# Kernel optimization log

Measured on AMD Instinct MI355X. Metric: run time of the kernel, lower is better.

Reference implementation:

```python
import jax, jax.numpy as jnp
import numpy as np

B, S_DIM, A_DIM = 8192, 39, 4
D_IN = S_DIM + A_DIM  # 43
F = 1024              # n_features width
E = 8                 # n_experts
C = 10                # n_contexts
N_OUT = 1


def setup_inputs() -> dict:
    key = jax.random.key(0)
    ks = jax.random.split(key, 12)
    inp = {
        "state": jax.random.normal(ks[0], (B, S_DIM), jnp.float32),
        "action": jax.random.normal(ks[1], (B, A_DIM), jnp.float32),
        "c": jax.random.randint(ks[2], (B,), 0, C, jnp.int32),
        # per-expert backbone params (InputLayer+ParallelLayer => E independent MLPs)
        "W0": jax.random.normal(ks[3], (E, D_IN, F), jnp.float32) * 0.05,
        "b0": jnp.zeros((E, F), jnp.float32),
        "W1": jax.random.normal(ks[4], (E, F, F), jnp.float32) * 0.03,
        "b1": jnp.zeros((E, F), jnp.float32),
        # task encoder: Linear(n_contexts -> n_experts, bias=False), weight [E, C]
        "Wte": jax.random.normal(ks[5], (E, C), jnp.float32) * 0.3,
        # per-context output heads: Linear(F -> 1)
        "Wh": jax.random.normal(ks[6], (C, F, N_OUT), jnp.float32) * 0.03,
        "bh": jnp.zeros((C, N_OUT), jnp.float32),
    }
    return inp


def reference(state, action, c, W0, b0, W1, b1, Wte, Wh, bh):
    # mixture weights: one_hot(c) @ Wte^T  ==  Wte[:, c]^T  -> [B, E]
    w = Wte.T[c]                                            # [B, E]
    sa = jnp.concatenate([state, action], axis=1)           # [B, D_IN]
    # per-expert backbone MLP (ReLU after each layer, incl. last since activation='ReLU')
    h = jax.nn.relu(jnp.einsum('bi,eio->ebo', sa, W0) + b0[:, None, :])   # [E, B, F]
    h = jax.nn.relu(jnp.einsum('ebi,eio->ebo', h, W1) + b1[:, None, :])   # [E, B, F]
    feats = jnp.transpose(h, (1, 0, 2))                     # [B, E, F]
    feats = jax.nn.relu(feats)                              # agg_activation[0]
    mixed = jnp.einsum('be,bef->bf', w, feats)              # [B, F]
    mixed = jax.nn.relu(mixed)                              # agg_activation[1]
    # context-routed heads: gather each sample's head params (same math as the
    # unique-context scatter loop in the original)
    q = jnp.einsum('bf,bfo->bo', mixed, Wh[c]) + bh[c]      # [B, 1]
    return jnp.squeeze(q, axis=-1)                          # [B]
```

## Files before the change

kernel.cpp:

```cpp
#include <hip/hip_runtime.h>
#include <hip/hip_bf16.h>
#include <stdint.h>

typedef __attribute__((ext_vector_type(8))) __bf16 bf16x8;
typedef __attribute__((ext_vector_type(4))) float f32x4;

__device__ __forceinline__ unsigned short f2b(float f) {
    return __builtin_bit_cast(unsigned short, __float2bfloat16(f));
}

__device__ __forceinline__ void gload_lds16(const void* g, void* l) {
    __builtin_amdgcn_global_load_lds(
        (__attribute__((address_space(1))) void*)(uintptr_t)g,
        (__attribute__((address_space(3))) void*)l,
        16, 0, 0);
}

#define MFMA16(a, b, c) __builtin_amdgcn_mfma_f32_16x16x32_bf16((a), (b), (c), 0, 0, 0)


__global__ void k_prep_sa(const float* __restrict__ state, const float* __restrict__ action,
                          const int* __restrict__ c, const float* __restrict__ Wte,
                          unsigned short* __restrict__ SA, float* __restrict__ wmix, int B) {
    int b = blockIdx.x * 256 + threadIdx.x;
    if (b >= B) return;
    unsigned short* row = SA + (size_t)b * 64;
#pragma unroll
    for (int i = 0; i < 39; ++i) row[i] = f2b(state[(size_t)b * 39 + i]);
#pragma unroll
    for (int i = 0; i < 4; ++i) row[39 + i] = f2b(action[(size_t)b * 4 + i]);
#pragma unroll
    for (int i = 43; i < 64; ++i) row[i] = 0;
    int ctx = c[b];
#pragma unroll
    for (int e = 0; e < 8; ++e) wmix[(size_t)b * 8 + e] = Wte[e * 10 + ctx];
}

__global__ void k_prep_w0t(const float* __restrict__ W0, unsigned short* __restrict__ W0T) {
    int idx = blockIdx.x * 256 + threadIdx.x;
    int e = idx >> 10, f = idx & 1023;
    unsigned short* dst = W0T + (size_t)idx * 64;
#pragma unroll 1
    for (int k = 0; k < 43; ++k) dst[k] = f2b(W0[((size_t)e * 43 + k) * 1024 + f]);
#pragma unroll
    for (int k = 43; k < 64; ++k) dst[k] = 0;
}

__global__ void k_prep_w1t(const float* __restrict__ W1, unsigned short* __restrict__ W1T) {
    __shared__ float t[64][65];
    int k0 = blockIdx.x * 64, n0 = blockIdx.y * 64, e = blockIdx.z;
    int tid = threadIdx.x;
    int cl = tid & 63;
    int rg = tid >> 6;
    const float* src = W1 + ((size_t)e * 1024 + k0) * 1024 + n0;
#pragma unroll
    for (int i = 0; i < 16; ++i) {
        int kr = rg * 16 + i;
        t[kr][cl] = src[(size_t)kr * 1024 + cl];
    }
    __syncthreads();
    int nl = tid >> 2, kg = tid & 3;
    unsigned short* dst = W1T + ((size_t)e * 1024 + n0 + nl) * 1024 + k0 + kg * 16;
#pragma unroll
    for (int j = 0; j < 16; ++j) dst[j] = f2b(t[kg * 16 + j][nl]);
}

__global__ __launch_bounds__(256, 2)
void k_layer0(const unsigned short* __restrict__ SA,
              const unsigned short* __restrict__ W0T,
              const float* __restrict__ b0,
              unsigned short* __restrict__ H0,
              int Bc, int row0) {
    __shared__ unsigned short As[128 * 64];
    __shared__ unsigned short Bs[128 * 64];
    int bm = blockIdx.x, bn = blockIdx.y, e = blockIdx.z;
    int tid = threadIdx.x, lane = tid & 63;
    int wv = tid >> 6, wr = wv >> 1, wc = wv & 1;
    int l15 = lane & 15, kg = lane >> 4;

    const char* Ag = (const char*)(SA + (size_t)(row0 + bm * 128) * 64);
    const char* Bg = (const char*)(W0T + ((size_t)e * 1024 + bn * 128) * 64);
#pragma unroll
    for (int it = 0; it < 4; ++it) {
        int off = tid * 16 + it * 4096;
        gload_lds16(Ag + off, (char*)As + off);
        gload_lds16(Bg + off, (char*)Bs + off);
    }
    __syncthreads();

    f32x4 acc[4][4];
#pragma unroll
    for (int mi = 0; mi < 4; ++mi)
#pragma unroll
        for (int ni = 0; ni < 4; ++ni) acc[mi][ni] = (f32x4)0.0f;

#pragma unroll
    for (int ks = 0; ks < 2; ++ks) {
        bf16x8 af[4], bv[4];
#pragma unroll
        for (int mi = 0; mi < 4; ++mi)
            af[mi] = *(const bf16x8*)&As[(wr * 64 + mi * 16 + l15) * 64 + ks * 32 + kg * 8];
#pragma unroll
        for (int ni = 0; ni < 4; ++ni)
            bv[ni] = *(const bf16x8*)&Bs[(wc * 64 + ni * 16 + l15) * 64 + ks * 32 + kg * 8];
#pragma unroll
        for (int mi = 0; mi < 4; ++mi)
#pragma unroll
            for (int ni = 0; ni < 4; ++ni)
                acc[mi][ni] = MFMA16(af[mi], bv[ni], acc[mi][ni]);
    }

    float b0v[4];
#pragma unroll
    for (int ni = 0; ni < 4; ++ni)
        b0v[ni] = b0[e * 1024 + bn * 128 + wc * 64 + ni * 16 + l15];
#pragma unroll
    for (int mi = 0; mi < 4; ++mi)
#pragma unroll
        for (int ni = 0; ni < 4; ++ni)
#pragma unroll
            for (int j = 0; j < 4; ++j) {
                int rloc = bm * 128 + wr * 64 + mi * 16 + kg * 4 + j;
                int col = bn * 128 + wc * 64 + ni * 16 + l15;
                float h = fmaxf(acc[mi][ni][j] + b0v[ni], 0.0f);
                H0[((size_t)e * Bc + rloc) * 1024 + col] = f2b(h);
            }
}

__global__ __launch_bounds__(512, 2)
void k_layer1_mix(const unsigned short* __restrict__ H0,
                  const unsigned short* __restrict__ W1T,
                  const float* __restrict__ b1,
                  const float* __restrict__ wmix,
                  float* __restrict__ mixed,
                  int Bc, int row0) {
    __shared__ unsigned short As[2][256 * 64];
    __shared__ unsigned short Bs[2][128 * 64];
    __shared__ float wmixLds[256 * 8];
    __shared__ float b1Lds[8 * 128];

    int nwg = (Bc / 256) * 8;
    int wg = blockIdx.x;
    int cpx = nwg >> 3;
    int swz = (wg & 7) * cpx + (wg >> 3);
    int bm = swz >> 3, bn = swz & 7;

    int tid = threadIdx.x, lane = tid & 63;
    int wv = tid >> 6;
    int wr = wv >> 1, wc = wv & 1;
    int l15 = lane & 15, kg = lane >> 4;

    int tid16 = tid * 16;
    int aSrc[4], aDst[4], bSrc[2], bDst[2];
#pragma unroll
    for (int i = 0; i < 4; ++i) {
        int flat = tid16 + i * 8192;
        int row = flat >> 7, colb = flat & 127;
        aDst[i] = flat;
        aSrc[i] = row * 2048 + (colb ^ ((row & 7) << 4));
    }
#pragma unroll
    for (int i = 0; i < 2; ++i) {
        int flat = tid16 + i * 8192;
        int row = flat >> 7, colb = flat & 127;
        bDst[i] = flat;
        bSrc[i] = row * 2048 + (colb ^ ((row & 7) << 4));
    }

    const char* h0base = (const char*)H0 + (size_t)(bm * 256) * 2048;
    const char* w1base = (const char*)W1T + (size_t)(bn * 128) * 2048;
    size_t eAstride = (size_t)Bc * 2048;

    int xsw = (l15 & 7) << 4;
    int aRow[4], bRow[4];
#pragma unroll
    for (int mi = 0; mi < 4; ++mi) aRow[mi] = (wr * 64 + mi * 16 + l15) * 128;
#pragma unroll
    for (int ni = 0; ni < 4; ++ni) bRow[ni] = (wc * 64 + ni * 16 + l15) * 128;
    int kg16 = kg * 16;

    for (int idx = tid; idx < 2048; idx += 512) {
        int r = idx >> 3, e = idx & 7;
        wmixLds[idx] = wmix[(size_t)(row0 + bm * 256 + r) * 8 + e];
    }
#pragma unroll
    for (int idx = tid; idx < 1024; idx += 512)
        b1Lds[idx] = b1[(idx >> 7) * 1024 + bn * 128 + (idx & 127)];
    __syncthreads();

    f32x4 acc[4][4], mix[4][4];
#pragma unroll
    for (int mi = 0; mi < 4; ++mi)
#pragma unroll
        for (int ni = 0; ni < 4; ++ni) { acc[mi][ni] = (f32x4)0.0f; mix[mi][ni] = (f32x4)0.0f; }

    const int NT = 128;

    auto STAGE = [&](int tt) {
        int e = tt >> 4;
        int k0b = (tt & 15) << 7;
        const char* Ab = h0base + (size_t)e * eAstride + k0b;
        const char* Bb = w1base + (size_t)e * (1024 * 2048) + k0b;
        char* Ad = (char*)As[tt & 1];
        char* Bd = (char*)Bs[tt & 1];
#pragma unroll
        for (int i = 0; i < 4; ++i) gload_lds16(Ab + aSrc[i], Ad + aDst[i]);
#pragma unroll
        for (int i = 0; i < 2; ++i) gload_lds16(Bb + bSrc[i], Bd + bDst[i]);
    };

    STAGE(0);

    for (int t = 0; t < NT; ++t) {
        if (t + 1 < NT) {
            STAGE(t + 1);
            asm volatile("s_waitcnt vmcnt(6)\n\ts_barrier" ::: "memory");
        } else {
            asm volatile("s_waitcnt vmcnt(0)\n\ts_barrier" ::: "memory");
        }
        __builtin_amdgcn_sched_barrier(0);

        const char* Ab = (const char*)As[t & 1];
        const char* Bb = (const char*)Bs[t & 1];

        __builtin_amdgcn_s_setprio(1);
#pragma unroll
        for (int ks = 0; ks < 2; ++ks) {
            int kb = (ks * 64 + kg16) ^ xsw;
            bf16x8 af[4], bv[4];
#pragma unroll
            for (int mi = 0; mi < 4; ++mi) af[mi] = *(const bf16x8*)(Ab + aRow[mi] + kb);
#pragma unroll
            for (int ni = 0; ni < 4; ++ni) bv[ni] = *(const bf16x8*)(Bb + bRow[ni] + kb);
#pragma unroll
            for (int mi = 0; mi < 4; ++mi)
#pragma unroll
                for (int ni = 0; ni < 4; ++ni)
                    acc[mi][ni] = MFMA16(af[mi], bv[ni], acc[mi][ni]);
        }
        __builtin_amdgcn_s_setprio(0);
        __builtin_amdgcn_sched_barrier(0);
        asm volatile("s_waitcnt lgkmcnt(0)\n\ts_barrier" ::: "memory");

        if ((t & 15) == 15) {
            int e = t >> 4;
            float b1v[4];
#pragma unroll
            for (int ni = 0; ni < 4; ++ni)
                b1v[ni] = b1Lds[e * 128 + wc * 64 + ni * 16 + l15];
#pragma unroll
            for (int mi = 0; mi < 4; ++mi)
#pragma unroll
                for (int j = 0; j < 4; ++j) {
                    int lrow = wr * 64 + mi * 16 + kg * 4 + j;
                    float w = wmixLds[lrow * 8 + e];
#pragma unroll
                    for (int ni = 0; ni < 4; ++ni) {
                        float h = fmaxf(acc[mi][ni][j] + b1v[ni], 0.0f);
                        mix[mi][ni][j] += w * h;
                        acc[mi][ni][j] = 0.0f;
                    }
                }
        }
    }

#pragma unroll
    for (int mi = 0; mi < 4; ++mi)
#pragma unroll
        for (int ni = 0; ni < 4; ++ni)
#pragma unroll
            for (int j = 0; j < 4; ++j) {
                int lrow = wr * 64 + mi * 16 + kg * 4 + j;
                int col = bn * 128 + wc * 64 + ni * 16 + l15;
                mixed[(size_t)(bm * 256 + lrow) * 1024 + col] = fmaxf(mix[mi][ni][j], 0.0f);
            }
}

__global__ void k_head(const float* __restrict__ mixed, const float* __restrict__ Wh,
                       const float* __restrict__ bh, const int* __restrict__ c,
                       float* __restrict__ q, int Bc, int row0) {
    int row = blockIdx.x * 4 + (threadIdx.x >> 6);
    int lane = threadIdx.x & 63;
    if (row >= Bc) return;
    int grow = row0 + row;
    int ctx = c[grow];
    const float4* m4 = (const float4*)(mixed + (size_t)row * 1024);
    const float4* w4 = (const float4*)(Wh + (size_t)ctx * 1024);
    float s = 0.0f;
#pragma unroll
    for (int i = 0; i < 4; ++i) {
        float4 a = m4[lane + i * 64];
        float4 b = w4[lane + i * 64];
        s += a.x * b.x + a.y * b.y + a.z * b.z + a.w * b.w;
    }
#pragma unroll
    for (int off = 32; off > 0; off >>= 1) s += __shfl_down(s, off);
    if (lane == 0) q[grow] = s + bh[ctx];
}

extern "C" void kernel_launch(void* const* d_in, const int* in_sizes, int n_in,
                              void* d_out, int out_size, void* d_ws, size_t ws_size,
                              hipStream_t stream) {
    const float* state  = (const float*)d_in[0];
    const float* action = (const float*)d_in[1];
    const int*   c      = (const int*)d_in[2];
    const float* W0     = (const float*)d_in[3];
    const float* b0     = (const float*)d_in[4];
    const float* W1     = (const float*)d_in[5];
    const float* b1     = (const float*)d_in[6];
    const float* Wte    = (const float*)d_in[7];
    const float* Wh     = (const float*)d_in[8];
    const float* bh     = (const float*)d_in[9];
    float* q = (float*)d_out;
    int B = in_sizes[2];

    char* p = (char*)d_ws;
    unsigned short* W1T = (unsigned short*)p; p += (size_t)8 * 1024 * 1024 * 2;
    unsigned short* W0T = (unsigned short*)p; p += (size_t)8 * 1024 * 64 * 2;
    unsigned short* SA  = (unsigned short*)p; p += (size_t)B * 64 * 2;
    float* wmix         = (float*)p;          p += (size_t)B * 8 * 4;
    size_t fixed = (size_t)(p - (char*)d_ws);

    int Bc = B;
    while (Bc > 256 && fixed + (size_t)Bc * (8 * 1024 * 2 + 1024 * 4) > ws_size) Bc >>= 1;

    unsigned short* H0 = (unsigned short*)p; p += (size_t)8 * Bc * 1024 * 2;
    float* mixed       = (float*)p;

    k_prep_sa<<<(B + 255) / 256, 256, 0, stream>>>(state, action, c, Wte, SA, wmix, B);
    k_prep_w0t<<<(8 * 1024) / 256, 256, 0, stream>>>(W0, W0T);
    k_prep_w1t<<<dim3(16, 16, 8), 256, 0, stream>>>(W1, W1T);

    for (int row0 = 0; row0 < B; row0 += Bc) {
        k_layer0<<<dim3(Bc / 128, 8, 8), 256, 0, stream>>>(SA, W0T, b0, H0, Bc, row0);
        k_layer1_mix<<<(Bc / 256) * 8, 512, 0, stream>>>(H0, W1T, b1, wmix, mixed, Bc, row0);
        k_head<<<(Bc + 3) / 4, 256, 0, stream>>>(mixed, Wh, bh, c, q, Bc, row0);
    }
}
```

Measured before the change: 233.6 us.

## Remap waves to 2x4 layout and split tile loads into interleaved phases

Changes the wave layout from 4x2 (64x64 per wave) to 2x4 (128x32 per wave). The stage loads are split into two groups, and the second half of A is issued mid-iteration, so global-to-LDS copies overlap with MFMA phases. Each phase now loads only a few A fragments and waits before its MFMAs, with a barrier per phase. The goal is to cut register pressure and expose load latency less, at the cost of more barriers and more A-fragment LDS reads per wave.

```diff
diff --git a/kernel.cpp b/kernel.cpp
--- a/kernel.cpp
+++ b/kernel.cpp
@@ -147,8 +147,10 @@
 
     int tid = threadIdx.x, lane = tid & 63;
     int wv = tid >> 6;
-    int wr = wv >> 1, wc = wv & 1;
+    int wr = wv >> 2, wc = wv & 3;
     int l15 = lane & 15, kg = lane >> 4;
+    int kg16 = kg * 16;
+    int xsw = (l15 & 7) << 4;
 
     int tid16 = tid * 16;
     int aSrc[4], aDst[4], bSrc[2], bDst[2];
@@ -171,108 +173,142 @@
     const char* w1base = (const char*)W1T + (size_t)(bn * 128) * 2048;
     size_t eAstride = (size_t)Bc * 2048;
 
-    int xsw = (l15 & 7) << 4;
-    int aRow[4], bRow[4];
-#pragma unroll
-    for (int mi = 0; mi < 4; ++mi) aRow[mi] = (wr * 64 + mi * 16 + l15) * 128;
-#pragma unroll
-    for (int ni = 0; ni < 4; ++ni) bRow[ni] = (wc * 64 + ni * 16 + l15) * 128;
-    int kg16 = kg * 16;
+    int aOff[8], bOff[2];
+#pragma unroll
+    for (int m = 0; m < 8; ++m) aOff[m] = (wr * 128 + m * 16 + l15) * 128;
+#pragma unroll
+    for (int n = 0; n < 2; ++n) bOff[n] = (wc * 32 + n * 16 + l15) * 128;
 
     for (int idx = tid; idx < 2048; idx += 512) {
         int r = idx >> 3, e = idx & 7;
         wmixLds[idx] = wmix[(size_t)(row0 + bm * 256 + r) * 8 + e];
     }
-#pragma unroll
     for (int idx = tid; idx < 1024; idx += 512)
         b1Lds[idx] = b1[(idx >> 7) * 1024 + bn * 128 + (idx & 127)];
     __syncthreads();
 
-    f32x4 acc[4][4], mix[4][4];
-#pragma unroll
-    for (int mi = 0; mi < 4; ++mi)
-#pragma unroll
-        for (int ni = 0; ni < 4; ++ni) { acc[mi][ni] = (f32x4)0.0f; mix[mi][ni] = (f32x4)0.0f; }
+    f32x4 acc[8][2], mix[8][2];
+#pragma unroll
+    for (int m = 0; m < 8; ++m)
+#pragma unroll
+        for (int n = 0; n < 2; ++n) { acc[m][n] = (f32x4)0.0f; mix[m][n] = (f32x4)0.0f; }
 
     const int NT = 128;
 
-    auto STAGE = [&](int tt) {
+    auto STAGE_G0 = [&](int tt) {
         int e = tt >> 4;
         int k0b = (tt & 15) << 7;
         const char* Ab = h0base + (size_t)e * eAstride + k0b;
         const char* Bb = w1base + (size_t)e * (1024 * 2048) + k0b;
         char* Ad = (char*)As[tt & 1];
         char* Bd = (char*)Bs[tt & 1];
-#pragma unroll
-        for (int i = 0; i < 4; ++i) gload_lds16(Ab + aSrc[i], Ad + aDst[i]);
-#pragma unroll
-        for (int i = 0; i < 2; ++i) gload_lds16(Bb + bSrc[i], Bd + bDst[i]);
+        gload_lds16(Bb + bSrc[0], Bd + bDst[0]);
+        gload_lds16(Bb + bSrc[1], Bd + bDst[1]);
+        gload_lds16(Ab + aSrc[0], Ad + aDst[0]);
+        gload_lds16(Ab + aSrc[2], Ad + aDst[2]);
     };
-
-    STAGE(0);
-
+    auto STAGE_G1 = [&](int tt) {
+        int e = tt >> 4;
+        int k0b = (tt & 15) << 7;
+        const char* Ab = h0base + (size_t)e * eAstride + k0b;
+        char* Ad = (char*)As[tt & 1];
+        gload_lds16(Ab + aSrc[1], Ad + aDst[1]);
+        gload_lds16(Ab + aSrc[3], Ad + aDst[3]);
+    };
+
+#define KB0 ((0 * 64 + kg16) ^ xsw)
+#define KB1 ((1 * 64 + kg16) ^ xsw)
+
+#define PHASE(M0, M1)                                                       \
+    {                                                                       \
+        bf16x8 a00 = *(const bf16x8*)(Ab + aOff[M0] + KB0);                 \
+        bf16x8 a01 = *(const bf16x8*)(Ab + aOff[M0] + KB1);                 \
+        bf16x8 a10 = *(const bf16x8*)(Ab + aOff[M1] + KB0);                 \
+        bf16x8 a11 = *(const bf16x8*)(Ab + aOff[M1] + KB1);                 \
+        asm volatile("s_waitcnt lgkmcnt(0)" ::: "memory");                  \
+        __builtin_amdgcn_sched_barrier(0);                                  \
+        __builtin_amdgcn_s_setprio(1);                                      \
+        acc[M0][0] = MFMA16(a00, bf00, acc[M0][0]);                         \
+        acc[M0][1] = MFMA16(a00, bf10, acc[M0][1]);                         \
+        acc[M1][0] = MFMA16(a10, bf00, acc[M1][0]);                         \
+        acc[M1][1] = MFMA16(a10, bf10, acc[M1][1]);                         \
+        acc[M0][0] = MFMA16(a01, bf01, acc[M0][0]);                         \
+        acc[M0][1] = MFMA16(a01, bf11, acc[M0][1]);                         \
+        acc[M1][0] = MFMA16(a11, bf01, acc[M1][0]);                         \
+        acc[M1][1] = MFMA16(a11, bf11, acc[M1][1]);                         \
+        __builtin_amdgcn_s_setprio(0);                                      \
+        __builtin_amdgcn_sched_barrier(0);                                  \
+        asm volatile("s_barrier" ::: "memory");                             \
+    }
+
+    STAGE_G0(0);
+    STAGE_G1(0);
+
+#pragma unroll 1
     for (int t = 0; t < NT; ++t) {
+        const char* Ab = (const char*)As[t & 1];
+        const char* Bb = (const char*)Bs[t & 1];
+
         if (t + 1 < NT) {
-            STAGE(t + 1);
+            STAGE_G0(t + 1);
+            asm volatile("s_waitcnt vmcnt(6)\n\ts_barrier" ::: "memory");
+        } else {
+            asm volatile("s_waitcnt vmcnt(2)\n\ts_barrier" ::: "memory");
+        }
+        __builtin_amdgcn_sched_barrier(0);
+        bf16x8 bf00 = *(const bf16x8*)(Bb + bOff[0] + KB0);
+        bf16x8 bf01 = *(const bf16x8*)(Bb + bOff[0] + KB1);
+        bf16x8 bf10 = *(const bf16x8*)(Bb + bOff[1] + KB0);
+        bf16x8 bf11 = *(const bf16x8*)(Bb + bOff[1] + KB1);
+        PHASE(0, 1)
+
+        PHASE(2, 3)
+
+        if (t + 1 < NT) {
+            STAGE_G1(t + 1);
             asm volatile("s_waitcnt vmcnt(6)\n\ts_barrier" ::: "memory");
         } else {
             asm volatile("s_waitcnt vmcnt(0)\n\ts_barrier" ::: "memory");
         }
         __builtin_amdgcn_sched_barrier(0);
-
-        const char* Ab = (const char*)As[t & 1];
-        const char* Bb = (const char*)Bs[t & 1];
-
-        __builtin_amdgcn_s_setprio(1);
-#pragma unroll
-        for (int ks = 0; ks < 2; ++ks) {
-            int kb = (ks * 64 + kg16) ^ xsw;
-            bf16x8 af[4], bv[4];
-#pragma unroll
-            for (int mi = 0; mi < 4; ++mi) af[mi] = *(const bf16x8*)(Ab + aRow[mi] + kb);
-#pragma unroll
-            for (int ni = 0; ni < 4; ++ni) bv[ni] = *(const bf16x8*)(Bb + bRow[ni] + kb);
-#pragma unroll
-            for (int mi = 0; mi < 4; ++mi)
-#pragma unroll
-                for (int ni = 0; ni < 4; ++ni)
-                    acc[mi][ni] = MFMA16(af[mi], bv[ni], acc[mi][ni]);
-        }
-        __builtin_amdgcn_s_setprio(0);
-        __builtin_amdgcn_sched_barrier(0);
-        asm volatile("s_waitcnt lgkmcnt(0)\n\ts_barrier" ::: "memory");
+        PHASE(4, 5)
+
+        PHASE(6, 7)
 
         if ((t & 15) == 15) {
             int e = t >> 4;
-            float b1v[4];
-#pragma unroll
-            for (int ni = 0; ni < 4; ++ni)
-                b1v[ni] = b1Lds[e * 128 + wc * 64 + ni * 16 + l15];
-#pragma unroll
-            for (int mi = 0; mi < 4; ++mi)
+            float b1v[2];
+#pragma unroll
+            for (int n = 0; n < 2; ++n)
+                b1v[n] = b1Lds[e * 128 + wc * 32 + n * 16 + l15];
+#pragma unroll
+            for (int m = 0; m < 8; ++m)
 #pragma unroll
                 for (int j = 0; j < 4; ++j) {
-                    int lrow = wr * 64 + mi * 16 + kg * 4 + j;
+                    int lrow = wr * 128 + m * 16 + kg * 4 + j;
                     float w = wmixLds[lrow * 8 + e];
 #pragma unroll
-                    for (int ni = 0; ni < 4; ++ni) {
-                        float h = fmaxf(acc[mi][ni][j] + b1v[ni], 0.0f);
-                        mix[mi][ni][j] += w * h;
-                        acc[mi][ni][j] = 0.0f;
+                    for (int n = 0; n < 2; ++n) {
+                        float h = fmaxf(acc[m][n][j] + b1v[n], 0.0f);
+                        mix[m][n][j] += w * h;
+                        acc[m][n][j] = 0.0f;
                     }
                 }
         }
     }
-
-#pragma unroll
-    for (int mi = 0; mi < 4; ++mi)
-#pragma unroll
-        for (int ni = 0; ni < 4; ++ni)
+#undef PHASE
+#undef KB0
+#undef KB1
+
+#pragma unroll
+    for (int m = 0; m < 8; ++m)
+#pragma unroll
+        for (int n = 0; n < 2; ++n)
 #pragma unroll
             for (int j = 0; j < 4; ++j) {
-                int lrow = wr * 64 + mi * 16 + kg * 4 + j;
-                int col = bn * 128 + wc * 64 + ni * 16 + l15;
-                mixed[(size_t)(bm * 256 + lrow) * 1024 + col] = fmaxf(mix[mi][ni][j], 0.0f);
+                int lrow = wr * 128 + m * 16 + kg * 4 + j;
+                int col = bn * 128 + wc * 32 + n * 16 + l15;
+                mixed[(size_t)(bm * 256 + lrow) * 1024 + col] = fmaxf(mix[m][n][j], 0.0f);
             }
 }
 
```

After: 291.5 us. 24.7% more time.

## Split experts into two groups with 256x256 tiles and bf16 partial mixes

Applied to the files above, without the earlier changes.

The layer-1 GEMM now uses 256x256 output tiles, and the 8 experts are split into two groups of 4, each handled by a different workgroup. Each group writes a bf16 partial mixture, and the head kernel sums the two partials, applies ReLU and does the dot product. The goal is more data reuse per tile (fewer global loads of H0 and W1T per FLOP) and a half-width intermediate. Global loads are split into two halves interleaved with the MFMA blocks. Costs are higher register pressure (128 accumulators plus 128 mix floats per thread) at 512 threads, which may cut occupancy or spill, and bf16 rounding of the partial sums.

```diff
diff --git a/kernel.cpp b/kernel.cpp
--- a/kernel.cpp
+++ b/kernel.cpp
@@ -7,6 +7,9 @@
 
 __device__ __forceinline__ unsigned short f2b(float f) {
     return __builtin_bit_cast(unsigned short, __float2bfloat16(f));
+}
+__device__ __forceinline__ float b2f(unsigned int u) {
+    return __builtin_bit_cast(float, u << 16);
 }
 
 __device__ __forceinline__ void gload_lds16(const void* g, void* l) {
@@ -50,8 +53,7 @@
     __shared__ float t[64][65];
     int k0 = blockIdx.x * 64, n0 = blockIdx.y * 64, e = blockIdx.z;
     int tid = threadIdx.x;
-    int cl = tid & 63;
-    int rg = tid >> 6;
+    int cl = tid & 63, rg = tid >> 6;
     const float* src = W1 + ((size_t)e * 1024 + k0) * 1024 + n0;
 #pragma unroll
     for (int i = 0; i < 16; ++i) {
@@ -132,166 +134,200 @@
                   const unsigned short* __restrict__ W1T,
                   const float* __restrict__ b1,
                   const float* __restrict__ wmix,
-                  float* __restrict__ mixed,
+                  unsigned short* __restrict__ mixedP,
                   int Bc, int row0) {
     __shared__ unsigned short As[2][256 * 64];
-    __shared__ unsigned short Bs[2][128 * 64];
-    __shared__ float wmixLds[256 * 8];
-    __shared__ float b1Lds[8 * 128];
-
-    int nwg = (Bc / 256) * 8;
+    __shared__ unsigned short Bs[2][256 * 64];
+    __shared__ float wmixLds[256 * 4];
+    __shared__ float b1Lds[4 * 256];
+
+    int nbm = Bc / 256;
+    int P = nbm * 2;
     int wg = blockIdx.x;
-    int cpx = nwg >> 3;
-    int swz = (wg & 7) * cpx + (wg >> 3);
-    int bm = swz >> 3, bn = swz & 7;
+    int bm, bn, g;
+    if ((P & 7) == 0) {
+        int c8 = wg & 7, j = wg >> 3;
+        int p = c8 + 8 * (j >> 2);
+        bn = j & 3;
+        bm = p >> 1; g = p & 1;
+    } else {
+        bn = wg & 3; g = (wg >> 2) & 1; bm = wg >> 3;
+    }
 
     int tid = threadIdx.x, lane = tid & 63;
     int wv = tid >> 6;
-    int wr = wv >> 1, wc = wv & 1;
+    int wr = wv >> 2, wc = wv & 3;
     int l15 = lane & 15, kg = lane >> 4;
+    int kg16 = kg * 16;
+    int xsw = (l15 & 7) << 4;
 
     int tid16 = tid * 16;
-    int aSrc[4], aDst[4], bSrc[2], bDst[2];
+    int sSrc[4], sDst[4];
 #pragma unroll
     for (int i = 0; i < 4; ++i) {
         int flat = tid16 + i * 8192;
         int row = flat >> 7, colb = flat & 127;
-        aDst[i] = flat;
-        aSrc[i] = row * 2048 + (colb ^ ((row & 7) << 4));
-    }
-#pragma unroll
-    for (int i = 0; i < 2; ++i) {
-        int flat = tid16 + i * 8192;
-        int row = flat >> 7, colb = flat & 127;
-        bDst[i] = flat;
-        bSrc[i] = row * 2048 + (colb ^ ((row & 7) << 4));
+        sDst[i] = flat;
+        sSrc[i] = row * 2048 + (colb ^ ((row & 7) << 4));
     }
 
     const char* h0base = (const char*)H0 + (size_t)(bm * 256) * 2048;
-    const char* w1base = (const char*)W1T + (size_t)(bn * 128) * 2048;
+    const char* w1base = (const char*)W1T + (size_t)(bn * 256) * 2048;
     size_t eAstride = (size_t)Bc * 2048;
 
-    int xsw = (l15 & 7) << 4;
-    int aRow[4], bRow[4];
-#pragma unroll
-    for (int mi = 0; mi < 4; ++mi) aRow[mi] = (wr * 64 + mi * 16 + l15) * 128;
-#pragma unroll
-    for (int ni = 0; ni < 4; ++ni) bRow[ni] = (wc * 64 + ni * 16 + l15) * 128;
-    int kg16 = kg * 16;
-
-    for (int idx = tid; idx < 2048; idx += 512) {
-        int r = idx >> 3, e = idx & 7;
-        wmixLds[idx] = wmix[(size_t)(row0 + bm * 256 + r) * 8 + e];
-    }
-#pragma unroll
+    int aOff[8], bOff[4];
+#pragma unroll
+    for (int m = 0; m < 8; ++m) aOff[m] = (wr * 128 + m * 16 + l15) * 128;
+#pragma unroll
+    for (int n = 0; n < 4; ++n) bOff[n] = (wc * 64 + n * 16 + l15) * 128;
+
+    for (int idx = tid; idx < 1024; idx += 512) {
+        int r = idx >> 2, el = idx & 3;
+        wmixLds[idx] = wmix[(size_t)(row0 + bm * 256 + r) * 8 + g * 4 + el];
+    }
     for (int idx = tid; idx < 1024; idx += 512)
-        b1Lds[idx] = b1[(idx >> 7) * 1024 + bn * 128 + (idx & 127)];
-    __syncthreads();
-
-    f32x4 acc[4][4], mix[4][4];
-#pragma unroll
-    for (int mi = 0; mi < 4; ++mi)
-#pragma unroll
-        for (int ni = 0; ni < 4; ++ni) { acc[mi][ni] = (f32x4)0.0f; mix[mi][ni] = (f32x4)0.0f; }
-
-    const int NT = 128;
-
-    auto STAGE = [&](int tt) {
-        int e = tt >> 4;
+        b1Lds[idx] = b1[(g * 4 + (idx >> 8)) * 1024 + bn * 256 + (idx & 255)];
+
+    f32x4 acc[8], acc2[8];
+    f32x4 A0[8][4];
+    float mix[8][4][4];
+#pragma unroll
+    for (int m = 0; m < 8; ++m)
+#pragma unroll
+        for (int n = 0; n < 4; ++n) {
+            A0[m][n] = (f32x4)0.0f;
+#pragma unroll
+            for (int j = 0; j < 4; ++j) mix[m][n][j] = 0.0f;
+        }
+    (void)acc; (void)acc2;
+
+    const int NT = 64;
+
+    auto STAGE_G = [&](int tt, int half) {
+        int el = tt >> 4;
         int k0b = (tt & 15) << 7;
-        const char* Ab = h0base + (size_t)e * eAstride + k0b;
-        const char* Bb = w1base + (size_t)e * (1024 * 2048) + k0b;
+        const char* Ab = h0base + (size_t)(g * 4 + el) * eAstride + k0b;
+        const char* Bb = w1base + (size_t)(g * 4 + el) * (1024 * 2048) + k0b;
         char* Ad = (char*)As[tt & 1];
         char* Bd = (char*)Bs[tt & 1];
-#pragma unroll
-        for (int i = 0; i < 4; ++i) gload_lds16(Ab + aSrc[i], Ad + aDst[i]);
-#pragma unroll
-        for (int i = 0; i < 2; ++i) gload_lds16(Bb + bSrc[i], Bd + bDst[i]);
+        int i0 = half * 2;
+        gload_lds16(Ab + sSrc[i0], Ad + sDst[i0]);
+        gload_lds16(Ab + sSrc[i0 + 1], Ad + sDst[i0 + 1]);
+        gload_lds16(Bb + sSrc[i0], Bd + sDst[i0]);
+        gload_lds16(Bb + sSrc[i0 + 1], Bd + sDst[i0 + 1]);
     };
 
-    STAGE(0);
-
+    STAGE_G(0, 0);
+    STAGE_G(0, 1);
+    __syncthreads();
+
+#pragma unroll 1
     for (int t = 0; t < NT; ++t) {
-        if (t + 1 < NT) {
-            STAGE(t + 1);
-            asm volatile("s_waitcnt vmcnt(6)\n\ts_barrier" ::: "memory");
-        } else {
-            asm volatile("s_waitcnt vmcnt(0)\n\ts_barrier" ::: "memory");
-        }
-        __builtin_amdgcn_sched_barrier(0);
-
         const char* Ab = (const char*)As[t & 1];
         const char* Bb = (const char*)Bs[t & 1];
 
-        __builtin_amdgcn_s_setprio(1);
-#pragma unroll
-        for (int ks = 0; ks < 2; ++ks) {
-            int kb = (ks * 64 + kg16) ^ xsw;
-            bf16x8 af[4], bv[4];
-#pragma unroll
-            for (int mi = 0; mi < 4; ++mi) af[mi] = *(const bf16x8*)(Ab + aRow[mi] + kb);
-#pragma unroll
-            for (int ni = 0; ni < 4; ++ni) bv[ni] = *(const bf16x8*)(Bb + bRow[ni] + kb);
-#pragma unroll
-            for (int mi = 0; mi < 4; ++mi)
-#pragma unroll
-                for (int ni = 0; ni < 4; ++ni)
-                    acc[mi][ni] = MFMA16(af[mi], bv[ni], acc[mi][ni]);
-        }
-        __builtin_amdgcn_s_setprio(0);
-        __builtin_amdgcn_sched_barrier(0);
-        asm volatile("s_waitcnt lgkmcnt(0)\n\ts_barrier" ::: "memory");
+        {
+            int kb = kg16 ^ xsw;
+            bf16x8 af[8], bf[4];
+#pragma unroll
+            for (int m = 0; m < 8; ++m) af[m] = *(const bf16x8*)(Ab + aOff[m] + kb);
+#pragma unroll
+            for (int n = 0; n < 4; ++n) bf[n] = *(const bf16x8*)(Bb + bOff[n] + kb);
+            if (t + 1 < NT) STAGE_G(t + 1, 0);
+            asm volatile("s_waitcnt lgkmcnt(0)" ::: "memory");
+            __builtin_amdgcn_sched_barrier(0);
+            __builtin_amdgcn_s_setprio(1);
+#pragma unroll
+            for (int m = 0; m < 8; ++m)
+#pragma unroll
+                for (int n = 0; n < 4; ++n)
+                    A0[m][n] = MFMA16(af[m], bf[n], A0[m][n]);
+            __builtin_amdgcn_s_setprio(0);
+            __builtin_amdgcn_sched_barrier(0);
+        }
+        {
+            int kb = (64 + kg16) ^ xsw;
+            bf16x8 af[8], bf[4];
+#pragma unroll
+            for (int m = 0; m < 8; ++m) af[m] = *(const bf16x8*)(Ab + aOff[m] + kb);
+#pragma unroll
+            for (int n = 0; n < 4; ++n) bf[n] = *(const bf16x8*)(Bb + bOff[n] + kb);
+            if (t + 1 < NT) STAGE_G(t + 1, 1);
+            asm volatile("s_waitcnt lgkmcnt(0)" ::: "memory");
+            __builtin_amdgcn_sched_barrier(0);
+            __builtin_amdgcn_s_setprio(1);
+#pragma unroll
+            for (int m = 0; m < 8; ++m)
+#pragma unroll
+                for (int n = 0; n < 4; ++n)
+                    A0[m][n] = MFMA16(af[m], bf[n], A0[m][n]);
+            __builtin_amdgcn_s_setprio(0);
+            __builtin_amdgcn_sched_barrier(0);
+        }
+        asm volatile("s_waitcnt vmcnt(0)\n\ts_barrier" ::: "memory");
 
         if ((t & 15) == 15) {
-            int e = t >> 4;
+            int el = t >> 4;
             float b1v[4];
 #pragma unroll
-            for (int ni = 0; ni < 4; ++ni)
-                b1v[ni] = b1Lds[e * 128 + wc * 64 + ni * 16 + l15];
-#pragma unroll
-            for (int mi = 0; mi < 4; ++mi)
+            for (int n = 0; n < 4; ++n)
+                b1v[n] = b1Lds[el * 256 + wc * 64 + n * 16 + l15];
+#pragma unroll
+            for (int m = 0; m < 8; ++m)
 #pragma unroll
                 for (int j = 0; j < 4; ++j) {
-                    int lrow = wr * 64 + mi * 16 + kg * 4 + j;
-                    float w = wmixLds[lrow * 8 + e];
-#pragma unroll
-                    for (int ni = 0; ni < 4; ++ni) {
-                        float h = fmaxf(acc[mi][ni][j] + b1v[ni], 0.0f);
-                        mix[mi][ni][j] += w * h;
-                        acc[mi][ni][j] = 0.0f;
+                    int lrow = wr * 128 + m * 16 + kg * 4 + j;
+                    float w = wmixLds[lrow * 4 + el];
+#pragma unroll
+                    for (int n = 0; n < 4; ++n) {
+                        float h = fmaxf(A0[m][n][j] + b1v[n], 0.0f);
+                        mix[m][n][j] += w * h;
+                        A0[m][n][j] = 0.0f;
                     }
                 }
         }
     }
 
-#pragma unroll
-    for (int mi = 0; mi < 4; ++mi)
-#pragma unroll
-        for (int ni = 0; ni < 4; ++ni)
+    unsigned short* outp = mixedP + (size_t)g * Bc * 1024;
+#pragma unroll
+    for (int m = 0; m < 8; ++m)
+#pragma unroll
+        for (int n = 0; n < 4; ++n)
 #pragma unroll
             for (int j = 0; j < 4; ++j) {
-                int lrow = wr * 64 + mi * 16 + kg * 4 + j;
-                int col = bn * 128 + wc * 64 + ni * 16 + l15;
-                mixed[(size_t)(bm * 256 + lrow) * 1024 + col] = fmaxf(mix[mi][ni][j], 0.0f);
+                int lrow = wr * 128 + m * 16 + kg * 4 + j;
+                int col = bn * 256 + wc * 64 + n * 16 + l15;
+                outp[(size_t)(bm * 256 + lrow) * 1024 + col] = f2b(mix[m][n][j]);
             }
 }
 
-__global__ void k_head(const float* __restrict__ mixed, const float* __restrict__ Wh,
-                       const float* __restrict__ bh, const int* __restrict__ c,
-                       float* __restrict__ q, int Bc, int row0) {
+__global__ void k_head(const unsigned short* __restrict__ mixedP,
+                       const float* __restrict__ Wh, const float* __restrict__ bh,
+                       const int* __restrict__ c, float* __restrict__ q,
+                       int Bc, int row0) {
     int row = blockIdx.x * 4 + (threadIdx.x >> 6);
     int lane = threadIdx.x & 63;
     if (row >= Bc) return;
     int grow = row0 + row;
     int ctx = c[grow];
-    const float4* m4 = (const float4*)(mixed + (size_t)row * 1024);
-    const float4* w4 = (const float4*)(Wh + (size_t)ctx * 1024);
+    const unsigned short* pa = mixedP + (size_t)row * 1024 + lane * 16;
+    const unsigned short* pb = mixedP + (size_t)Bc * 1024 + (size_t)row * 1024 + lane * 16;
+    const float* wv = Wh + (size_t)ctx * 1024 + lane * 16;
     float s = 0.0f;
 #pragma unroll
-    for (int i = 0; i < 4; ++i) {
-        float4 a = m4[lane + i * 64];
-        float4 b = w4[lane + i * 64];
-        s += a.x * b.x + a.y * b.y + a.z * b.z + a.w * b.w;
+    for (int ch = 0; ch < 2; ++ch) {
+        uint4 ua = *(const uint4*)(pa + ch * 8);
+        uint4 ub = *(const uint4*)(pb + ch * 8);
+        const float* w8 = wv + ch * 8;
+        unsigned int au[4] = {ua.x, ua.y, ua.z, ua.w};
+        unsigned int bu[4] = {ub.x, ub.y, ub.z, ub.w};
+#pragma unroll
+        for (int i = 0; i < 4; ++i) {
+            float a0 = b2f(au[i] & 0xffffu), a1 = b2f(au[i] >> 16);
+            float c0 = b2f(bu[i] & 0xffffu), c1 = b2f(bu[i] >> 16);
+            s += fmaxf(a0 + c0, 0.0f) * w8[i * 2];
+            s += fmaxf(a1 + c1, 0.0f) * w8[i * 2 + 1];
+        }
     }
 #pragma unroll
     for (int off = 32; off > 0; off >>= 1) s += __shfl_down(s, off);
@@ -322,10 +358,10 @@
     size_t fixed = (size_t)(p - (char*)d_ws);
 
     int Bc = B;
-    while (Bc > 256 && fixed + (size_t)Bc * (8 * 1024 * 2 + 1024 * 4) > ws_size) Bc >>= 1;
-
-    unsigned short* H0 = (unsigned short*)p; p += (size_t)8 * Bc * 1024 * 2;
-    float* mixed       = (float*)p;
+    while (Bc > 256 && fixed + (size_t)Bc * (8 * 1024 * 2 + 2 * 1024 * 2) > ws_size) Bc >>= 1;
+
+    unsigned short* H0     = (unsigned short*)p; p += (size_t)8 * Bc * 1024 * 2;
+    unsigned short* mixedP = (unsigned short*)p;
 
     k_prep_sa<<<(B + 255) / 256, 256, 0, stream>>>(state, action, c, Wte, SA, wmix, B);
     k_prep_w0t<<<(8 * 1024) / 256, 256, 0, stream>>>(W0, W0T);
@@ -333,7 +369,7 @@
 
     for (int row0 = 0; row0 < B; row0 += Bc) {
         k_layer0<<<dim3(Bc / 128, 8, 8), 256, 0, stream>>>(SA, W0T, b0, H0, Bc, row0);
-        k_layer1_mix<<<(Bc / 256) * 8, 512, 0, stream>>>(H0, W1T, b1, wmix, mixed, Bc, row0);
-        k_head<<<(Bc + 3) / 4, 256, 0, stream>>>(mixed, Wh, bh, c, q, Bc, row0);
-    }
-}
+        k_layer1_mix<<<(Bc / 256) * 8, 512, 0, stream>>>(H0, W1T, b1, wmix, mixedP, Bc, row0);
+        k_head<<<(Bc + 3) / 4, 256, 0, stream>>>(mixedP, Wh, bh, c, q, Bc, row0);
+    }
+}
```

Result: slower. 281.7 us (+20.6%).
